# Optimization experiments

Hardware: AMD Instinct MI355X
Metric: run time of the kernel (lower is better)

## Reference

```python
import jax, jax.numpy as jnp
import numpy as np

VOCAB = 32000
D = 256        # embedding dim
NB = 256       # n_bubbles
NEQ = 5        # n_equilibrium_steps
THRESH = 1.5   # surprise_threshold
SEQ = 64
DECAYS = np.array([0.3, 0.7, 0.9], dtype=np.float32)  # RunningKnow frame decay rates


def setup_inputs() -> dict:
    key = jax.random.key(0)
    k1, k2, k3 = jax.random.split(key, 3)
    tokens = jax.random.randint(k1, (SEQ,), 0, VOCAB)
    E = jax.random.normal(k2, (VOCAB, D), dtype=jnp.float32)
    # Foam bubble measurement operators (stand-in: per-bubble linear map), scaled for sane stats
    W = jax.random.normal(k3, (NB, D, D), dtype=jnp.float32) / np.float32(np.sqrt(D))
    return {
        "tokens": tokens,
        "E": E,
        "W": W,
        "memory_decay_base": jnp.asarray(0.8, dtype=jnp.float32),
        "novelty_sensitivity": jnp.asarray(1.0, dtype=jnp.float32),
    }


def _equilibrate(m):
    # Stand-in for Foam.equilibrate: NEQ relaxation steps toward the bubble mean.
    for _ in range(NEQ):
        m = m + 0.1 * (m.mean(axis=0, keepdims=True) - m)
    return m


def reference(tokens, E, W, memory_decay_base, novelty_sensitivity):
    dr = jnp.asarray(DECAYS)[:, None, None]          # [F,1,1]
    F = dr.shape[0]
    sens = jnp.abs(novelty_sensitivity)

    def step(carry, tok):
        memory, means, vars_, n_seen = carry
        x = E[tok]                                   # [D]
        mm = memory.mean(axis=0)                     # [D]
        mem_norm = jnp.linalg.norm(mm) + 1e-10
        x_norm = jnp.linalg.norm(x) + 1e-10
        novelty = jnp.where(mem_norm > 1e-8,
                            1.0 - jnp.dot(x, mm) / (x_norm * mem_norm),
                            jnp.float32(1.0))
        decay = jax.nn.sigmoid(memory_decay_base - sens * novelty)
        xm = x + decay * mm                          # [D]

        meas = jnp.einsum('d,nde->ne', xm, W)        # [NB,D] bubble measurements

        # RunningKnow.evaluate (blank model at n_seen==0 -> never knows)
        std = jnp.sqrt(vars_ + 1e-8)                 # [F,NB,D]
        surprise = (jnp.abs(meas[None] - means) / std).mean(axis=(1, 2))  # [F]
        any_knows = jnp.any((surprise < THRESH) & (n_seen > 0))

        eq = _equilibrate(meas)
        eff = jnp.where(any_knows, meas, eq)         # know -> skip equilibration
        eff_d = jax.lax.stop_gradient(eff)           # .detach() in torch

        # RunningKnow.update (EMA mean/var per frame; first call initializes)
        upd_mean = dr * means + (1.0 - dr) * eff_d
        upd_var = jnp.maximum(dr * vars_ + (1.0 - dr) * (eff_d - means) * (eff_d - upd_mean), 1e-8)
        first = (n_seen == 0)
        means = jnp.where(first, jnp.broadcast_to(eff_d, (F, NB, D)), upd_mean)
        vars_ = jnp.where(first, jnp.float32(0.1), upd_var)

        # density matrix and spectrum
        mnorm = eff / (jnp.linalg.norm(eff, axis=-1, keepdims=True) + 1e-10)  # [NB,D]
        rho = mnorm.T @ mnorm / NB                   # [D,D]
        eigs = jnp.linalg.eigvalsh(jax.lax.stop_gradient(rho))
        eigs = jnp.maximum(eigs, 1e-12)
        eigs = eigs / eigs.sum()

        memory = decay * memory + (1.0 - decay) * eff_d
        logits = ((E @ rho) * E).sum(axis=-1)        # [VOCAB]
        return (memory, means, vars_, n_seen + 1), (logits, eigs)

    carry0 = (jnp.zeros((NB, D), jnp.float32),
              jnp.zeros((F, NB, D), jnp.float32),
              jnp.ones((F, NB, D), jnp.float32),
              jnp.int32(0))
    _, (logits, eigs) = jax.lax.scan(step, carry0, tokens)
    return logits, eigs  # [SEQ,VOCAB], [SEQ,D]
```

## Files before the change

kernel.cpp:

```cpp
#include <hip/hip_runtime.h>
#include <hip/hip_bf16.h>
#include <cstdint>
#include <cstddef>

constexpr size_t OFF_MEM    = 0;
constexpr size_t OFF_XM     = 65536;
constexpr size_t OFF_MU     = 82176;
constexpr size_t OFF_SABS   = 98560;
constexpr size_t OFF_BAR    = 98816;
constexpr size_t ZERO_END   = 98880;
constexpr size_t OFF_WBAR   = 98880;
constexpr size_t OFF_MEANS  = 164416;
constexpr size_t OFF_VARS   = 361024;
constexpr size_t OFF_DT     = 557632;
constexpr size_t OFF_ET     = 574016;
constexpr size_t OFF_RHO    = 590400;
constexpr size_t OFF_MN16   = 4784704;
constexpr size_t OFF_E16    = 6881856;
constexpr size_t WS_FLOATS  = 10977856;

#define SEQ_ 64
#define VOCAB_ 32000

typedef __attribute__((ext_vector_type(8))) short bf16x8;
typedef __attribute__((ext_vector_type(4))) float f32x4;

__device__ __forceinline__ float wave_sum(float v){
  v += __shfl_xor(v, 32); v += __shfl_xor(v, 16); v += __shfl_xor(v, 8);
  v += __shfl_xor(v, 4);  v += __shfl_xor(v, 2);  v += __shfl_xor(v, 1);
  return v;
}
__device__ __forceinline__ float block_sum(float v, float* red){
  int tid = threadIdx.x;
  v = wave_sum(v);
  if ((tid & 63) == 0) red[tid >> 6] = v;
  __syncthreads();
  float r = red[0] + red[1] + red[2] + red[3];
  __syncthreads();
  return r;
}

__global__ __launch_bounds__(256) void k0_init(const float* __restrict__ E, float* __restrict__ ws){
  size_t i = (size_t)blockIdx.x * 256 + threadIdx.x;
  if (i < ZERO_END) ws[i] = 0.f;
  __hip_bfloat16* e16 = (__hip_bfloat16*)(ws + OFF_E16);
  e16[i] = __float2bfloat16(E[i]);
}

__global__ __launch_bounds__(256) void k_wbar(const float* __restrict__ W, float* __restrict__ ws){
  size_t i = (size_t)blockIdx.x * 256 + threadIdx.x;
  float s = 0.f;
  #pragma unroll 4
  for (int n = 0; n < 256; ++n)
    s += W[(size_t)n * 65536 + i];
  ws[OFF_WBAR + i] = s * (1.0f / 256.0f);
}

__global__ __launch_bounds__(1024, 1) void k_xm(const int* __restrict__ tokens,
    const float* __restrict__ E, const float* __restrict__ mdbp,
    const float* __restrict__ nsp, float* __restrict__ ws){
  __shared__ float xm_s[256];
  __shared__ __align__(16) float part[4][256];
  __shared__ float redA[16], redB[16], redC[16];
  const int tid = threadIdx.x;
  const int e = tid & 255, q = tid >> 8;
  const int lane = tid & 63, w = tid >> 6;
  const float sens = fabsf(nsp[0]);
  const float mdb  = mdbp[0];
  const float* Wb = ws + OFF_WBAR;
  float mm = 0.f;

  float wreg[64];
  {
    const float* Wq = Wb + (size_t)(q * 64) * 256 + e;
    #pragma unroll
    for (int dd = 0; dd < 64; ++dd)
      wreg[dd] = Wq[(size_t)dd * 256];
  }

  for (int t = 0; t < SEQ_; ++t){
    int tok = tokens[t];
    float xv = (tid < 256) ? E[(size_t)tok * 256 + e] : 0.f;
    float a = wave_sum(xv * mm);
    float b = wave_sum(xv * xv);
    float c = wave_sum(mm * mm);
    if (lane == 0){ redA[w] = a; redB[w] = b; redC[w] = c; }
    __syncthreads();
    float sdot = (redA[0] + redA[1]) + (redA[2] + redA[3]);
    float sx2  = (redB[0] + redB[1]) + (redB[2] + redB[3]);
    float sm2  = (redC[0] + redC[1]) + (redC[2] + redC[3]);
    float mem_norm = sqrtf(sm2) + 1e-10f;
    float x_norm   = sqrtf(sx2) + 1e-10f;
    float novelty = (mem_norm > 1e-8f) ? (1.0f - sdot / (x_norm * mem_norm)) : 1.0f;
    float z = mdb - sens * novelty;
    float decay = 1.0f / (1.0f + expf(-z));
    if (tid < 256){
      float xmv = xv + decay * mm;
      xm_s[e] = xmv;
      ws[OFF_XM + (size_t)e * 64 + t] = xmv;
    }
    __syncthreads();

    float p = 0.f;
    #pragma unroll
    for (int dd = 0; dd < 64; ++dd)
      p = fmaf(xm_s[q * 64 + dd], wreg[dd], p);
    part[q][e] = p;
    __syncthreads();
    if (tid < 256){
      float acc = (part[0][e] + part[1][e]) + (part[2][e] + part[3][e]);
      ws[OFF_MU + (size_t)t * 256 + e] = acc;
      mm = decay * mm + (1.0f - decay) * acc;
    }
    __syncthreads();
  }
}

__global__ __launch_bounds__(256) void k_measall(const float* __restrict__ W, float* __restrict__ ws){
  __shared__ __align__(16) float xm_s[16384];
  const int tid = threadIdx.x, n = blockIdx.x;
  for (int i = tid; i < 16384; i += 256) xm_s[i] = ws[OFF_XM + i];
  __syncthreads();

  float acc[64];
  #pragma unroll
  for (int t = 0; t < 64; ++t) acc[t] = 0.f;

  const float* Wn = W + (size_t)n * 65536 + tid;
  for (int d = 0; d < 256; ++d){
    float wv = Wn[(size_t)d * 256];
    const float* xr = &xm_s[d * 64];
    #pragma unroll
    for (int q = 0; q < 16; ++q){
      float4 x4 = *(const float4*)&xr[q * 4];
      acc[q * 4 + 0] = fmaf(x4.x, wv, acc[q * 4 + 0]);
      acc[q * 4 + 1] = fmaf(x4.y, wv, acc[q * 4 + 1]);
      acc[q * 4 + 2] = fmaf(x4.z, wv, acc[q * 4 + 2]);
      acc[q * 4 + 3] = fmaf(x4.w, wv, acc[q * 4 + 3]);
    }
  }
  #pragma unroll
  for (int t = 0; t < 64; ++t)
    ws[OFF_RHO + (size_t)n * 16384 + (size_t)t * 256 + tid] = acc[t];
}

__global__ __launch_bounds__(1024, 1) void k_stats(float* __restrict__ ws){
  __shared__ float redA[16], redB[16], redC[16];
  const int tid = threadIdx.x;
  const int e = tid & 255, q = tid >> 8;
  const int lane = tid & 63, w = tid >> 6;
  const int n = blockIdx.x * 4 + q;
  unsigned* bar = (unsigned*)(ws + OFF_BAR);
  __hip_bfloat16* mn16 = (__hip_bfloat16*)(ws + OFF_MN16);
  const size_t ne = (size_t)n * 256 + e;
  const float TH = 1.5f * 65536.0f;
  const float c5 = 0.59049f;

  float mean0 = 0.f, mean1 = 0.f, mean2 = 0.f;
  float var0 = 0.f, var1 = 0.f, var2 = 0.f;

  for (int t = 0; t < SEQ_; ++t){
    float me = ws[OFF_RHO + (size_t)n * 16384 + (size_t)t * 256 + e];
    bool know = false;
    if (t > 0){
      float v0 = fabsf(me - mean0) / sqrtf(var0 + 1e-8f);
      float v1 = fabsf(me - mean1) / sqrtf(var1 + 1e-8f);
      float v2 = fabsf(me - mean2) / sqrtf(var2 + 1e-8f);
      float a = wave_sum(v0), b = wave_sum(v1), c = wave_sum(v2);
      if (lane == 0){ redA[w] = a; redB[w] = b; redC[w] = c; }
      __syncthreads();
      if (tid == 0){
        float sA = 0.f, sB = 0.f, sC = 0.f;
        #pragma unroll
        for (int i = 0; i < 16; ++i){ sA += redA[i]; sB += redB[i]; sC += redC[i]; }
        atomicAdd(&ws[OFF_SABS + (size_t)t * 4 + 0], sA);
        atomicAdd(&ws[OFF_SABS + (size_t)t * 4 + 1], sB);
        atomicAdd(&ws[OFF_SABS + (size_t)t * 4 + 2], sC);
        __hip_atomic_fetch_add(bar, 1u, __ATOMIC_ACQ_REL, __HIP_MEMORY_SCOPE_AGENT);
        unsigned tgt = 64u * (unsigned)t;
        while (__hip_atomic_load(bar, __ATOMIC_ACQUIRE, __HIP_MEMORY_SCOPE_AGENT) < tgt)
          __builtin_amdgcn_s_sleep(2);
      }
      __syncthreads();
      float s0 = __hip_atomic_load(&ws[OFF_SABS + (size_t)t * 4 + 0], __ATOMIC_RELAXED, __HIP_MEMORY_SCOPE_AGENT);
      float s1 = __hip_atomic_load(&ws[OFF_SABS + (size_t)t * 4 + 1], __ATOMIC_RELAXED, __HIP_MEMORY_SCOPE_AGENT);
      float s2 = __hip_atomic_load(&ws[OFF_SABS + (size_t)t * 4 + 2], __ATOMIC_RELAXED, __HIP_MEMORY_SCOPE_AGENT);
      know = (s0 < TH) || (s1 < TH) || (s2 < TH);
    }
    float mu = ws[OFF_MU + (size_t)t * 256 + e];
    float eq = c5 * me + (1.0f - c5) * mu;
    float eff = know ? me : eq;

    if (t == 0){
      mean0 = eff; mean1 = eff; mean2 = eff;
      var0 = 0.1f; var1 = 0.1f; var2 = 0.1f;
    } else {
      float um, uv;
      um = 0.3f * mean0 + 0.7f * eff;
      uv = 0.3f * var0 + 0.7f * (eff - mean0) * (eff - um);
      mean0 = um; var0 = fmaxf(uv, 1e-8f);
      um = 0.7f * mean1 + 0.3f * eff;
      uv = 0.7f * var1 + 0.3f * (eff - mean1) * (eff - um);
      mean1 = um; var1 = fmaxf(uv, 1e-8f);
      um = 0.9f * mean2 + 0.1f * eff;
      uv = 0.9f * var2 + 0.1f * (eff - mean2) * (eff - um);
      mean2 = um; var2 = fmaxf(uv, 1e-8f);
    }

    float nv = wave_sum(eff * eff);
    if (lane == 0) redA[w] = nv;
    __syncthreads();
    float nr2 = (redA[4 * q + 0] + redA[4 * q + 1]) + (redA[4 * q + 2] + redA[4 * q + 3]);
    float rn = sqrtf(nr2) + 1e-10f;
    mn16[(size_t)t * 65536 + ne] = __float2bfloat16(eff / rn);
    __syncthreads();
  }
}

__global__ __launch_bounds__(256) void k_rho(float* __restrict__ ws){
  const int t = blockIdx.x, rb = blockIdx.y, tid = threadIdx.x;
  __shared__ __align__(16) float tile[32][256];
  const unsigned short* mn16 = (const unsigned short*)(ws + OFF_MN16);
  float acc[32];
  #pragma unroll
  for (int i = 0; i < 32; ++i) acc[i] = 0.f;
  for (int c = 0; c < 8; ++c){
    __syncthreads();
    #pragma unroll
    for (int v = 0; v < 4; ++v){
      int idx = v * 256 + tid;
      int row = idx >> 5, c16 = idx & 31;
      uint4 u4 = *(const uint4*)(mn16 + (size_t)t * 65536 + (size_t)(c * 32 + row) * 256 + c16 * 8);
      float* dst = &tile[row][c16 * 8];
      unsigned uu[4] = {u4.x, u4.y, u4.z, u4.w};
      #pragma unroll
      for (int j = 0; j < 4; ++j){
        dst[j * 2 + 0] = __uint_as_float(uu[j] << 16);
        dst[j * 2 + 1] = __uint_as_float(uu[j] & 0xffff0000u);
      }
    }
    __syncthreads();
    for (int nl = 0; nl < 32; ++nl){
      float ev = tile[nl][tid];
      #pragma unroll
      for (int q = 0; q < 8; ++q){
        float4 dv = *(const float4*)&tile[nl][rb * 32 + q * 4];
        acc[q * 4 + 0] = fmaf(dv.x, ev, acc[q * 4 + 0]);
        acc[q * 4 + 1] = fmaf(dv.y, ev, acc[q * 4 + 1]);
        acc[q * 4 + 2] = fmaf(dv.z, ev, acc[q * 4 + 2]);
        acc[q * 4 + 3] = fmaf(dv.w, ev, acc[q * 4 + 3]);
      }
    }
  }
  #pragma unroll
  for (int i = 0; i < 32; ++i)
    ws[OFF_RHO + (size_t)t * 65536 + (size_t)(rb * 32 + i) * 256 + tid] = acc[i] * (1.0f / 256.0f);
}

__global__ __launch_bounds__(512, 2) void k_trigemm(float* __restrict__ ws, float* __restrict__ out){
  __shared__ __align__(16) char smem_raw[51200];
  const int tid = threadIdx.x;

  if (blockIdx.x < 64){
    float* ca   = (float*)smem_raw;
    float* ua   = ca + 256;
    float* wa   = ua + 256;
    float* ph   = wa + 256;
    float* redA = ph + 512;
    float* redB = redA + 8;
    float* dd   = redB + 8;
    float* ee   = dd + 256;
    const int t = blockIdx.x;
    const int c = tid & 255, h = tid >> 8;
    const int lane = tid & 63, w = tid >> 6;
    const float* rho = ws + OFF_RHO + (size_t)t * 65536;

    float Mreg[128];
    {
      const float* Mc = rho + (size_t)(h * 128) * 256 + c;
      #pragma unroll
      for (int rr = 0; rr < 128; ++rr)
        Mreg[rr] = Mc[(size_t)rr * 256];
    }
    const int rowbase = h * 128;

    for (int k = 0; k < 254; ++k){
      __syncthreads();
      if (c == k){
        #pragma unroll
        for (int rr = 0; rr < 128; ++rr) ca[rowbase + rr] = Mreg[rr];
      }
      __syncthreads();
      float uval = 0.f;
      if (tid < 256){
        float raw = ca[tid];
        uval = (tid > k) ? raw : 0.f;
        ua[tid] = uval;
        if (tid == 0) dd[k] = ca[k];
      }
      float pa = wave_sum(uval * uval);
      if ((tid & 63) == 0) redA[tid >> 6] = pa;
      __syncthreads();
      float sigma2 = redA[0] + redA[1] + redA[2] + redA[3]
                   + redA[4] + redA[5] + redA[6] + redA[7];
      float v0 = ca[k + 1];
      if (sigma2 < 1e-30f){
        if (tid == 0) ee[k] = v0;
        continue;
      }
      float sig = sqrtf(sigma2);
      float alpha = (v0 >= 0.f) ? -sig : sig;
      float u0 = v0 - alpha;
      float beta = 2.0f / (sigma2 - v0 * v0 + u0 * u0);
      if (tid == 0) ee[k] = alpha;
      if (tid == k + 1) ua[tid] = u0;
      __syncthreads();

      {
        float a0 = 0.f, a1 = 0.f, a2 = 0.f, a3 = 0.f;
        #pragma unroll
        for (int rr = 0; rr < 128; rr += 4){
          float4 u4 = *(const float4*)&ua[rowbase + rr];
          a0 = fmaf(Mreg[rr + 0], u4.x, a0);
          a1 = fmaf(Mreg[rr + 1], u4.y, a1);
          a2 = fmaf(Mreg[rr + 2], u4.z, a2);
          a3 = fmaf(Mreg[rr + 3], u4.w, a3);
        }
        ph[tid] = (a0 + a1) + (a2 + a3);
      }
      __syncthreads();
      float p = ph[c] + ph[c + 256];
      float up = (tid < 256) ? ua[tid] * p : 0.f;
      float pb = wave_sum(up);
      if ((tid & 63) == 0) redB[tid >> 6] = pb;
      __syncthreads();
      float s = redB[0] + redB[1] + redB[2] + redB[3]
              + redB[4] + redB[5] + redB[6] + redB[7];
      if (tid < 256) wa[tid] = (tid > k) ? (beta * p - 0.5f * beta * beta * s * ua[tid]) : 0.f;
      __syncthreads();
      {
        float ucv = ua[c], wcv = wa[c];
        #pragma unroll
        for (int rr = 0; rr < 128; rr += 4){
          float4 u4 = *(const float4*)&ua[rowbase + rr];
          float4 w4 = *(const float4*)&wa[rowbase + rr];
          Mreg[rr + 0] = fmaf(-w4.x, ucv, fmaf(-u4.x, wcv, Mreg[rr + 0]));
          Mreg[rr + 1] = fmaf(-w4.y, ucv, fmaf(-u4.y, wcv, Mreg[rr + 1]));
          Mreg[rr + 2] = fmaf(-w4.z, ucv, fmaf(-u4.z, wcv, Mreg[rr + 2]));
          Mreg[rr + 3] = fmaf(-w4.w, ucv, fmaf(-u4.w, wcv, Mreg[rr + 3]));
        }
      }
    }

    __syncthreads();
    if (c == 254){
      #pragma unroll
      for (int rr = 0; rr < 128; ++rr) ca[rowbase + rr] = Mreg[rr];
    }
    __syncthreads();
    if (tid == 0){ dd[254] = ca[254]; ee[254] = ca[255]; }
    __syncthreads();
    if (c == 255){
      #pragma unroll
      for (int rr = 0; rr < 128; ++rr) ca[rowbase + rr] = Mreg[rr];
    }
    __syncthreads();
    if (tid == 0){ dd[255] = ca[255]; ee[255] = 0.f; }
    __syncthreads();

    float dvv = dd[c];
    float evv = ee[c];
    if (h == 0){ ua[c] = evv * evv; ph[c] = fabsf(evv); }
    __syncthreads();
    float rad = ph[c] + ((c > 0) ? ph[c - 1] : 0.f);
    float vmin = dvv - rad, vmax = dvv + rad;
    vmin = fminf(vmin, __shfl_xor(vmin, 32)); vmin = fminf(vmin, __shfl_xor(vmin, 16));
    vmin = fminf(vmin, __shfl_xor(vmin, 8));  vmin = fminf(vmin, __shfl_xor(vmin, 4));
    vmin = fminf(vmin, __shfl_xor(vmin, 2));  vmin = fminf(vmin, __shfl_xor(vmin, 1));
    vmax = fmaxf(vmax, __shfl_xor(vmax, 32)); vmax = fmaxf(vmax, __shfl_xor(vmax, 16));
    vmax = fmaxf(vmax, __shfl_xor(vmax, 8));  vmax = fmaxf(vmax, __shfl_xor(vmax, 4));
    vmax = fmaxf(vmax, __shfl_xor(vmax, 2));  vmax = fmaxf(vmax, __shfl_xor(vmax, 1));
    if (lane == 0){ redA[w] = vmin; redB[w] = vmax; }
    __syncthreads();
    float glo = fminf(fminf(fminf(redA[0], redA[1]), fminf(redA[2], redA[3])),
                      fminf(fminf(redA[4], redA[5]), fminf(redA[6], redA[7])));
    float ghi = fmaxf(fmaxf(fmaxf(redB[0], redB[1]), fmaxf(redB[2], redB[3])),
                      fmaxf(fmaxf(redB[4], redB[5]), fmaxf(redB[6], redB[7])));
    __syncthreads();

    float lo = glo, hi = ghi;
    for (int it = 0; it < 40; ++it){
      float mid = 0.5f * (lo + hi);
      float qv = dd[0] - mid;
      int cnt = (qv < 0.f) ? 1 : 0;
      #pragma unroll 8
      for (int i = 1; i < 256; ++i){
        float qr = __builtin_amdgcn_rcpf(qv);
        qv = (dd[i] - mid) - ua[i - 1] * qr;
        qv = (fabsf(qv) < 1e-25f) ? -1e-25f : qv;
        cnt += (qv < 0.f) ? 1 : 0;
      }
      if (cnt <= c) lo = mid; else hi = mid;
    }
    float lam = fmaxf(0.5f * (lo + hi), 1e-12f);
    float lp = (h == 0) ? lam : 0.f;
    lp = wave_sum(lp);
    if (lane == 0) redA[w] = lp;
    __syncthreads();
    float ssum = ((redA[0] + redA[1]) + (redA[2] + redA[3]))
               + ((redA[4] + redA[5]) + (redA[6] + redA[7]));
    if (h == 0)
      out[(size_t)SEQ_ * VOCAB_ + (size_t)t * 256 + c] = lam / ssum;
  } else {
    short* A_lds = (short*)smem_raw;
    short* B_lds = A_lds + 8192;
    float* pl    = (float*)(B_lds + 16384);
    const int g = blockIdx.x - 64;
    const int bx = g % 250, t = g / 250;
    const int lane = tid & 63, w = tid >> 6;
    const int wr = w >> 2, wc = w & 3;
    const int vbase = bx * 128;
    const short* E16 = (const short*)(ws + OFF_E16);
    const short* MN  = (const short*)(ws + OFF_MN16) + (size_t)t * 65536;

    f32x4 acc[4][4];
    #pragma unroll
    for (int i = 0; i < 4; ++i)
      #pragma unroll
      for (int j = 0; j < 4; ++j){ f32x4 z = {0.f, 0.f, 0.f, 0.f}; acc[i][j] = z; }

    const int gq = lane >> 4, r16 = lane & 15;
    const int sx = r16 & 7;
    for (int it = 0; it < 4; ++it){
      const int k0 = it * 64;
      __syncthreads();
      #pragma unroll
      for (int pa = 0; pa < 2; ++pa){
        int ch = pa * 512 + tid;
        int row = ch >> 3, c8 = ch & 7;
        int sc8 = c8 ^ (row & 7);
        uint4 v = *(const uint4*)(E16 + (size_t)(vbase + row) * 256 + k0 + sc8 * 8);
        *(uint4*)&A_lds[ch * 8] = v;
      }
      #pragma unroll
      for (int pb = 0; pb < 4; ++pb){
        int ch = pb * 512 + tid;
        int row = ch >> 3, c8 = ch & 7;
        int sc8 = c8 ^ (row & 7);
        uint4 v = *(const uint4*)(MN + (size_t)row * 256 + k0 + sc8 * 8);
        *(uint4*)&B_lds[ch * 8] = v;
      }
      __syncthreads();
      #pragma unroll
      for (int kk = 0; kk < 64; kk += 32){
        const int j0 = (kk >> 3) + gq;
        bf16x8 af[4], bf[4];
        #pragma unroll
        for (int fm = 0; fm < 4; ++fm)
          af[fm] = *(const bf16x8*)&A_lds[(wr * 64 + fm * 16 + r16) * 64 + (j0 ^ sx) * 8];
        #pragma unroll
        for (int fn = 0; fn < 4; ++fn)
          bf[fn] = *(const bf16x8*)&B_lds[(wc * 64 + fn * 16 + r16) * 64 + (j0 ^ sx) * 8];
        #pragma unroll
        for (int fm = 0; fm < 4; ++fm)
          #pragma unroll
          for (int fn = 0; fn < 4; ++fn)
            acc[fm][fn] = __builtin_amdgcn_mfma_f32_16x16x32_bf16(af[fm], bf[fn], acc[fm][fn], 0, 0, 0);
      }
    }

    float ps[4][4];
    #pragma unroll
    for (int fm = 0; fm < 4; ++fm)
      #pragma unroll
      for (int i = 0; i < 4; ++i){
        float sv = 0.f;
        #pragma unroll
        for (int fn = 0; fn < 4; ++fn){ float v = acc[fm][fn][i]; sv += v * v; }
        sv += __shfl_xor(sv, 1); sv += __shfl_xor(sv, 2);
        sv += __shfl_xor(sv, 4); sv += __shfl_xor(sv, 8);
        ps[fm][i] = sv;
      }
    __syncthreads();
    if (r16 == 0){
      #pragma unroll
      for (int fm = 0; fm < 4; ++fm)
        #pragma unroll
        for (int i = 0; i < 4; ++i)
          pl[w * 64 + fm * 16 + gq * 4 + i] = ps[fm][i];
    }
    __syncthreads();
    if (tid < 128){
      int rr = tid;
      int wrr = rr >> 6, lr = rr & 63;
      float sum = pl[(wrr * 4 + 0) * 64 + lr] + pl[(wrr * 4 + 1) * 64 + lr]
                + pl[(wrr * 4 + 2) * 64 + lr] + pl[(wrr * 4 + 3) * 64 + lr];
      out[(size_t)t * VOCAB_ + vbase + rr] = sum * (1.0f / 256.0f);
    }
  }
}

extern "C" void kernel_launch(void* const* d_in, const int* in_sizes, int n_in,
                              void* d_out, int out_size, void* d_ws, size_t ws_size,
                              hipStream_t stream){
  const int*   tokens = (const int*)d_in[0];
  const float* E      = (const float*)d_in[1];
  const float* W      = (const float*)d_in[2];
  const float* mdbp   = (const float*)d_in[3];
  const float* nsp    = (const float*)d_in[4];
  float* out = (float*)d_out;
  float* ws  = (float*)d_ws;
  if (ws_size < WS_FLOATS * sizeof(float)) return;

  k0_init<<<dim3(32000), dim3(256), 0, stream>>>(E, ws);
  k_wbar<<<dim3(256), dim3(256), 0, stream>>>(W, ws);
  k_xm<<<dim3(1), dim3(1024), 0, stream>>>(tokens, E, mdbp, nsp, ws);
  k_measall<<<dim3(256), dim3(256), 0, stream>>>(W, ws);
  {
    void* args[1];
    args[0] = (void*)&ws;
    hipLaunchCooperativeKernel((const void*)k_stats, dim3(64), dim3(1024), args, 0, stream);
  }
  k_rho<<<dim3(64, 8), dim3(256), 0, stream>>>(ws);
  k_trigemm<<<dim3(64 + 250 * 64), dim3(512), 0, stream>>>(ws, out);
}
```

Before: 3.104 ms.

## Fold init into serial kernel, split tridiag and bisection blocks, replace atomics

Removes the separate init launch by running the E-to-bf16 conversion in extra blocks of the single-block k_xm kernel, so that conversion overlaps the serial recurrence. Zeroing of the barrier and flags moves into k_wbar. In k_stats, float atomicAdd accumulation is replaced by per-block partial stores that each block reads and wave-reduces, and two redundant block barriers are dropped. In k_trigemm, the tridiagonalization blocks now publish d/e to global memory and set a flag. Separate bisection blocks wait on that flag, which frees the Householder blocks earlier. The cost is spin-wait dependence between blocks of one launch and more scheduling complexity.

```diff
diff --git a/kernel.cpp b/kernel.cpp
--- a/kernel.cpp
+++ b/kernel.cpp
@@ -40,13 +40,6 @@
   return r;
 }
 
-__global__ __launch_bounds__(256) void k0_init(const float* __restrict__ E, float* __restrict__ ws){
-  size_t i = (size_t)blockIdx.x * 256 + threadIdx.x;
-  if (i < ZERO_END) ws[i] = 0.f;
-  __hip_bfloat16* e16 = (__hip_bfloat16*)(ws + OFF_E16);
-  e16[i] = __float2bfloat16(E[i]);
-}
-
 __global__ __launch_bounds__(256) void k_wbar(const float* __restrict__ W, float* __restrict__ ws){
   size_t i = (size_t)blockIdx.x * 256 + threadIdx.x;
   float s = 0.f;
@@ -54,11 +47,21 @@
   for (int n = 0; n < 256; ++n)
     s += W[(size_t)n * 65536 + i];
   ws[OFF_WBAR + i] = s * (1.0f / 256.0f);
+  if (blockIdx.x == 0){
+    if (threadIdx.x < 64) ((unsigned*)(ws + OFF_SABS))[threadIdx.x] = 0u;
+    if (threadIdx.x == 64) *(unsigned*)(ws + OFF_BAR) = 0u;
+  }
 }
 
 __global__ __launch_bounds__(1024, 1) void k_xm(const int* __restrict__ tokens,
     const float* __restrict__ E, const float* __restrict__ mdbp,
     const float* __restrict__ nsp, float* __restrict__ ws){
+  if (blockIdx.x != 0){
+    size_t i = (size_t)(blockIdx.x - 1) * 1024 + threadIdx.x;
+    __hip_bfloat16* e16 = (__hip_bfloat16*)(ws + OFF_E16);
+    e16[i] = __float2bfloat16(E[i]);
+    return;
+  }
   __shared__ float xm_s[256];
   __shared__ __align__(16) float part[4][256];
   __shared__ float redA[16], redB[16], redC[16];
@@ -112,7 +115,6 @@
       ws[OFF_MU + (size_t)t * 256 + e] = acc;
       mm = decay * mm + (1.0f - decay) * acc;
     }
-    __syncthreads();
   }
 }
 
@@ -145,12 +147,13 @@
 }
 
 __global__ __launch_bounds__(1024, 1) void k_stats(float* __restrict__ ws){
-  __shared__ float redA[16], redB[16], redC[16];
+  __shared__ float redA[16], redB[16], redC[16], redD[16];
   const int tid = threadIdx.x;
   const int e = tid & 255, q = tid >> 8;
   const int lane = tid & 63, w = tid >> 6;
   const int n = blockIdx.x * 4 + q;
   unsigned* bar = (unsigned*)(ws + OFF_BAR);
+  float* sabsP = ws + OFF_MEANS;
   __hip_bfloat16* mn16 = (__hip_bfloat16*)(ws + OFF_MN16);
   const size_t ne = (size_t)n * 256 + e;
   const float TH = 1.5f * 65536.0f;
@@ -173,18 +176,23 @@
         float sA = 0.f, sB = 0.f, sC = 0.f;
         #pragma unroll
         for (int i = 0; i < 16; ++i){ sA += redA[i]; sB += redB[i]; sC += redC[i]; }
-        atomicAdd(&ws[OFF_SABS + (size_t)t * 4 + 0], sA);
-        atomicAdd(&ws[OFF_SABS + (size_t)t * 4 + 1], sB);
-        atomicAdd(&ws[OFF_SABS + (size_t)t * 4 + 2], sC);
+        size_t base = (size_t)t * 192 + blockIdx.x;
+        __hip_atomic_store(&sabsP[base],       sA, __ATOMIC_RELAXED, __HIP_MEMORY_SCOPE_AGENT);
+        __hip_atomic_store(&sabsP[base + 64],  sB, __ATOMIC_RELAXED, __HIP_MEMORY_SCOPE_AGENT);
+        __hip_atomic_store(&sabsP[base + 128], sC, __ATOMIC_RELAXED, __HIP_MEMORY_SCOPE_AGENT);
         __hip_atomic_fetch_add(bar, 1u, __ATOMIC_ACQ_REL, __HIP_MEMORY_SCOPE_AGENT);
         unsigned tgt = 64u * (unsigned)t;
         while (__hip_atomic_load(bar, __ATOMIC_ACQUIRE, __HIP_MEMORY_SCOPE_AGENT) < tgt)
           __builtin_amdgcn_s_sleep(2);
       }
       __syncthreads();
-      float s0 = __hip_atomic_load(&ws[OFF_SABS + (size_t)t * 4 + 0], __ATOMIC_RELAXED, __HIP_MEMORY_SCOPE_AGENT);
-      float s1 = __hip_atomic_load(&ws[OFF_SABS + (size_t)t * 4 + 1], __ATOMIC_RELAXED, __HIP_MEMORY_SCOPE_AGENT);
-      float s2 = __hip_atomic_load(&ws[OFF_SABS + (size_t)t * 4 + 2], __ATOMIC_RELAXED, __HIP_MEMORY_SCOPE_AGENT);
+      size_t pbase = (size_t)t * 192;
+      float p0 = __hip_atomic_load(&sabsP[pbase + lane],       __ATOMIC_RELAXED, __HIP_MEMORY_SCOPE_AGENT);
+      float p1 = __hip_atomic_load(&sabsP[pbase + 64 + lane],  __ATOMIC_RELAXED, __HIP_MEMORY_SCOPE_AGENT);
+      float p2 = __hip_atomic_load(&sabsP[pbase + 128 + lane], __ATOMIC_RELAXED, __HIP_MEMORY_SCOPE_AGENT);
+      float s0 = wave_sum(p0);
+      float s1 = wave_sum(p1);
+      float s2 = wave_sum(p2);
       know = (s0 < TH) || (s1 < TH) || (s2 < TH);
     }
     float mu = ws[OFF_MU + (size_t)t * 256 + e];
@@ -208,12 +216,11 @@
     }
 
     float nv = wave_sum(eff * eff);
-    if (lane == 0) redA[w] = nv;
-    __syncthreads();
-    float nr2 = (redA[4 * q + 0] + redA[4 * q + 1]) + (redA[4 * q + 2] + redA[4 * q + 3]);
+    if (lane == 0) redD[w] = nv;
+    __syncthreads();
+    float nr2 = (redD[4 * q + 0] + redD[4 * q + 1]) + (redD[4 * q + 2] + redD[4 * q + 3]);
     float rn = sqrtf(nr2) + 1e-10f;
     mn16[(size_t)t * 65536 + ne] = __float2bfloat16(eff / rn);
-    __syncthreads();
   }
 }
 
@@ -268,12 +275,11 @@
     float* ph   = wa + 256;
     float* redA = ph + 512;
     float* redB = redA + 8;
-    float* dd   = redB + 8;
-    float* ee   = dd + 256;
     const int t = blockIdx.x;
     const int c = tid & 255, h = tid >> 8;
-    const int lane = tid & 63, w = tid >> 6;
     const float* rho = ws + OFF_RHO + (size_t)t * 65536;
+    float* dT = ws + OFF_DT + (size_t)t * 256;
+    float* eT = ws + OFF_ET + (size_t)t * 256;
 
     float Mreg[128];
     {
@@ -296,7 +302,7 @@
         float raw = ca[tid];
         uval = (tid > k) ? raw : 0.f;
         ua[tid] = uval;
-        if (tid == 0) dd[k] = ca[k];
+        if (tid == 0) dT[k] = ca[k];
       }
       float pa = wave_sum(uval * uval);
       if ((tid & 63) == 0) redA[tid >> 6] = pa;
@@ -305,14 +311,14 @@
                    + redA[4] + redA[5] + redA[6] + redA[7];
       float v0 = ca[k + 1];
       if (sigma2 < 1e-30f){
-        if (tid == 0) ee[k] = v0;
+        if (tid == 0) eT[k] = v0;
         continue;
       }
       float sig = sqrtf(sigma2);
       float alpha = (v0 >= 0.f) ? -sig : sig;
       float u0 = v0 - alpha;
       float beta = 2.0f / (sigma2 - v0 * v0 + u0 * u0);
-      if (tid == 0) ee[k] = alpha;
+      if (tid == 0) eT[k] = alpha;
       if (tid == k + 1) ua[tid] = u0;
       __syncthreads();
 
@@ -358,19 +364,39 @@
       for (int rr = 0; rr < 128; ++rr) ca[rowbase + rr] = Mreg[rr];
     }
     __syncthreads();
-    if (tid == 0){ dd[254] = ca[254]; ee[254] = ca[255]; }
+    if (tid == 0){ dT[254] = ca[254]; eT[254] = ca[255]; }
     __syncthreads();
     if (c == 255){
       #pragma unroll
       for (int rr = 0; rr < 128; ++rr) ca[rowbase + rr] = Mreg[rr];
     }
     __syncthreads();
-    if (tid == 0){ dd[255] = ca[255]; ee[255] = 0.f; }
-    __syncthreads();
-
-    float dvv = dd[c];
-    float evv = ee[c];
-    if (h == 0){ ua[c] = evv * evv; ph[c] = fabsf(evv); }
+    if (tid == 0){
+      dT[255] = ca[255]; eT[255] = 0.f;
+      __hip_atomic_store(((unsigned*)(ws + OFF_SABS)) + t, 1u,
+                         __ATOMIC_RELEASE, __HIP_MEMORY_SCOPE_AGENT);
+    }
+  } else if (blockIdx.x < 128){
+    float* ua   = (float*)smem_raw;
+    float* ph   = ua + 256;
+    float* dd   = ph + 256;
+    float* redA = dd + 256;
+    float* redB = redA + 8;
+    const int t = blockIdx.x - 64;
+    const int c = tid & 255, h = tid >> 8;
+    const int lane = tid & 63, w = tid >> 6;
+    unsigned* flag = (unsigned*)(ws + OFF_SABS);
+    if (tid == 0){
+      while (__hip_atomic_load(&flag[t], __ATOMIC_RELAXED, __HIP_MEMORY_SCOPE_AGENT) == 0u)
+        __builtin_amdgcn_s_sleep(8);
+    }
+    __syncthreads();
+    (void)__hip_atomic_load(&flag[t], __ATOMIC_ACQUIRE, __HIP_MEMORY_SCOPE_AGENT);
+    const float* dT = ws + OFF_DT + (size_t)t * 256;
+    const float* eT = ws + OFF_ET + (size_t)t * 256;
+    float dvv = dT[c];
+    float evv = eT[c];
+    if (h == 0){ dd[c] = dvv; ua[c] = evv * evv; ph[c] = fabsf(evv); }
     __syncthreads();
     float rad = ph[c] + ((c > 0) ? ph[c - 1] : 0.f);
     float vmin = dvv - rad, vmax = dvv + rad;
@@ -415,7 +441,7 @@
     short* A_lds = (short*)smem_raw;
     short* B_lds = A_lds + 8192;
     float* pl    = (float*)(B_lds + 16384);
-    const int g = blockIdx.x - 64;
+    const int g = blockIdx.x - 128;
     const int bx = g % 250, t = g / 250;
     const int lane = tid & 63, w = tid >> 6;
     const int wr = w >> 2, wc = w & 3;
@@ -512,9 +538,8 @@
   float* ws  = (float*)d_ws;
   if (ws_size < WS_FLOATS * sizeof(float)) return;
 
-  k0_init<<<dim3(32000), dim3(256), 0, stream>>>(E, ws);
   k_wbar<<<dim3(256), dim3(256), 0, stream>>>(W, ws);
-  k_xm<<<dim3(1), dim3(1024), 0, stream>>>(tokens, E, mdbp, nsp, ws);
+  k_xm<<<dim3(8001), dim3(1024), 0, stream>>>(tokens, E, mdbp, nsp, ws);
   k_measall<<<dim3(256), dim3(256), 0, stream>>>(W, ws);
   {
     void* args[1];
@@ -522,5 +547,5 @@
     hipLaunchCooperativeKernel((const void*)k_stats, dim3(64), dim3(1024), args, 0, stream);
   }
   k_rho<<<dim3(64, 8), dim3(256), 0, stream>>>(ws);
-  k_trigemm<<<dim3(64 + 250 * 64), dim3(512), 0, stream>>>(ws, out);
-}
+  k_trigemm<<<dim3(128 + 250 * 64), dim3(512), 0, stream>>>(ws, out);
+}
```

New measurement: 2.945 ms. 5.1% less time.
